# Kernel optimization log

Hardware: AMD Instinct MI355X
Metric: run time of the kernel (lower is better)

## Reference

```python
import jax, jax.numpy as jnp
import numpy as np

L, B, H, IN = 2, 32, 2048, 2048  # layers, batch, hidden, input (=hidden here)


def setup_inputs() -> dict:
    key = jax.random.key(0)
    ks = jax.random.split(key, 8)
    s = 0.02
    return {
        "h0": jax.random.normal(ks[0], (L, B, H), jnp.float32),
        "c0": jax.random.normal(ks[1], (L, B, H), jnp.float32),
        "W_ih": jax.random.normal(ks[2], (L, 4 * H, IN), jnp.float32) * s,
        "W_hh": jax.random.normal(ks[3], (L, 4 * H, H), jnp.float32) * s,
        "b_ih": jax.random.normal(ks[4], (L, 4 * H), jnp.float32) * s,
        "b_hh": jax.random.normal(ks[5], (L, 4 * H), jnp.float32) * s,
        "W_out": jax.random.normal(ks[6], (IN, H), jnp.float32) * s,
        "b_out": jax.random.normal(ks[7], (IN,), jnp.float32) * s,
        "seq_len": 128,
    }


def _lstm_cell(x, h, c, W_ih, W_hh, b_ih, b_hh):
    # gates: [B, 4H]; PyTorch LSTMCell gate order i, f, g, o
    gates = x @ W_ih.T + b_ih + h @ W_hh.T + b_hh
    i, f, g, o = jnp.split(gates, 4, axis=-1)
    c_new = jax.nn.sigmoid(f) * c + jax.nn.sigmoid(i) * jnp.tanh(g)
    h_new = jax.nn.sigmoid(o) * jnp.tanh(c_new)
    return h_new, c_new


def reference(h0, c0, W_ih, W_hh, b_ih, b_hh, W_out, b_out, seq_len):
    batch, hidden = h0.shape[1], h0.shape[2]
    x0 = jnp.zeros((batch, hidden), h0.dtype)

    def step(carry, _):
        x, h, c = carry  # h, c: [L, B, H]
        hs, cs = [], []
        inp = x
        for l in range(h.shape[0]):  # small fixed layer loop
            h_l, c_l = _lstm_cell(inp, h[l], c[l], W_ih[l], W_hh[l], b_ih[l], b_hh[l])
            hs.append(h_l)
            cs.append(c_l)
            inp = h_l
        last_h = hs[-1]
        x_next = last_h @ W_out.T + b_out  # projected feedback
        return (x_next, jnp.stack(hs), jnp.stack(cs)), last_h

    _, out_feats = jax.lax.scan(step, (x0, h0, c0), None, length=seq_len)
    return out_feats  # [seq_len, B, H] (stacked list of per-step top-layer h)
```

## Files before the change

kernel.cpp:

```cpp
#include <hip/hip_runtime.h>


typedef __attribute__((ext_vector_type(8))) short short8;
typedef __attribute__((ext_vector_type(4))) short short4v;
typedef __attribute__((ext_vector_type(4))) float f32x4;

#define MFMA16(a, b, c) __builtin_amdgcn_mfma_f32_16x16x32_bf16((a), (b), (c), 0, 0, 0)
#define GDMA(gp, lp)                                                        \
  __builtin_amdgcn_global_load_lds(                                         \
      (const __attribute__((address_space(1))) unsigned int*)(gp),          \
      (__attribute__((address_space(3))) unsigned int*)(lp), 16, 0, 0)

static constexpr int BATCH = 32;
static constexpr int HID = 2048;
static constexpr int NWG = 256;
static constexpr int NTHR = 512;
static constexpr int BH = BATCH * HID;
static constexpr size_t WMAT = (size_t)8192 * 2048;
static constexpr int LDS_WRING = 0;
static constexpr int LDS_ARING = 32768;
static constexpr int LDS_RED = 98304;
static constexpr int LDS_BYTES = 114688;

#define AT_ADD(p, v) __hip_atomic_fetch_add((p), (v), __ATOMIC_RELAXED, __HIP_MEMORY_SCOPE_AGENT)
#define AT_LD(p) __hip_atomic_load((p), __ATOMIC_RELAXED, __HIP_MEMORY_SCOPE_AGENT)
#define AT_ST(p, v) __hip_atomic_store((p), (v), __ATOMIC_RELAXED, __HIP_MEMORY_SCOPE_AGENT)

__device__ __forceinline__ unsigned short f2bf(float x) {
  unsigned u = __float_as_uint(x);
  u += 0x7FFFu + ((u >> 16) & 1u);
  return (unsigned short)(u >> 16);
}
__device__ __forceinline__ float sigm(float x) { return 1.f / (1.f + __expf(-x)); }
__device__ __forceinline__ float tanh_(float x) {
  float e = __expf(2.f * x);
  return 1.f - 2.f / (e + 1.f);
}

__global__ void cvt_bf16_k(const float* __restrict__ s, unsigned short* __restrict__ d,
                           long n4) {
  long i = blockIdx.x * (long)blockDim.x + threadIdx.x;
  long st = (long)gridDim.x * blockDim.x;
  for (; i < n4; i += st) {
    float4 v = ((const float4*)s)[i];
    short4v o;
    o.x = (short)f2bf(v.x); o.y = (short)f2bf(v.y);
    o.z = (short)f2bf(v.z); o.w = (short)f2bf(v.w);
    ((short4v*)d)[i] = o;
  }
}

__global__ void tcvt_k(const float* __restrict__ src, unsigned short* __restrict__ dst) {
  __shared__ float T[64][65];
  const int jb = blockIdx.x * 64, kb = blockIdx.y * 64;
  const int tid = threadIdx.x;
#pragma unroll
  for (int r = 0; r < 4; ++r) {
    const int row = r * 16 + (tid >> 4), c4 = (tid & 15) * 4;
    float4 v = *(const float4*)&src[(size_t)(jb + row) * 2048 + kb + c4];
    T[row][c4] = v.x; T[row][c4 + 1] = v.y; T[row][c4 + 2] = v.z; T[row][c4 + 3] = v.w;
  }
  __syncthreads();
#pragma unroll
  for (int r = 0; r < 4; ++r) {
    const int k = r * 16 + (tid >> 4), j4 = (tid & 15) * 4;
    short4v o;
    o.x = (short)f2bf(T[j4][k]);     o.y = (short)f2bf(T[j4 + 1][k]);
    o.z = (short)f2bf(T[j4 + 2][k]); o.w = (short)f2bf(T[j4 + 3][k]);
    *(short4v*)&dst[(size_t)(kb + k) * 2048 + jb + j4] = o;
  }
}

__global__ void gemm_pack_k(const unsigned short* __restrict__ A,
                            const unsigned short* __restrict__ Bt,
                            unsigned short* __restrict__ Wfp) {
  __shared__ __align__(16) unsigned short As[128][72], Bs[128][72];
  const int tid = threadIdx.x, wv = tid >> 6, lane = tid & 63;
  const int wm = wv >> 1, wn = wv & 1;
  const int g0 = blockIdx.x * 128, k0 = blockIdx.y * 128;
  f32x4 acc[4][4];
#pragma unroll
  for (int i = 0; i < 4; ++i)
#pragma unroll
    for (int j = 0; j < 4; ++j) acc[i][j] = (f32x4){0.f, 0.f, 0.f, 0.f};

  for (int kt = 0; kt < 32; ++kt) {
#pragma unroll
    for (int rr = 0; rr < 4; ++rr) {
      const int row = rr * 32 + (tid >> 3), c8 = (tid & 7) * 8;
      *(short8*)&As[row][c8] = *(const short8*)&A[(size_t)(g0 + row) * 2048 + kt * 64 + c8];
      *(short8*)&Bs[row][c8] = *(const short8*)&Bt[(size_t)(k0 + row) * 2048 + kt * 64 + c8];
    }
    __syncthreads();
#pragma unroll
    for (int kk = 0; kk < 2; ++kk) {
      short8 af[4], bf[4];
#pragma unroll
      for (int mi = 0; mi < 4; ++mi)
        af[mi] = *(const short8*)&As[wm * 64 + mi * 16 + (lane & 15)][kk * 32 + (lane >> 4) * 8];
#pragma unroll
      for (int ni = 0; ni < 4; ++ni)
        bf[ni] = *(const short8*)&Bs[wn * 64 + ni * 16 + (lane & 15)][kk * 32 + (lane >> 4) * 8];
#pragma unroll
      for (int mi = 0; mi < 4; ++mi)
#pragma unroll
        for (int ni = 0; ni < 4; ++ni)
          acc[mi][ni] = MFMA16(af[mi], bf[ni], acc[mi][ni]);
    }
    __syncthreads();
  }
#pragma unroll
  for (int mi = 0; mi < 4; ++mi)
#pragma unroll
    for (int ni = 0; ni < 4; ++ni)
#pragma unroll
      for (int r = 0; r < 4; ++r) {
        const int g = g0 + wm * 64 + mi * 16 + (lane >> 4) * 4 + r;
        const int k = k0 + wn * 64 + ni * 16 + (lane & 15);
        const int gateblk = g >> 11, gcol = g & 2047;
        const int wgp = gcol >> 3, nn = (gcol & 7) + 8 * (gateblk & 1), tile = gateblk >> 1;
        const int kblk = k >> 5, e = k & 7, lane_p = nn + 16 * ((k >> 3) & 3);
        Wfp[(((size_t)(wgp * 2 + tile) * 64 + kblk) * 64 + lane_p) * 8 + e] =
            f2bf(acc[mi][ni][r]);
      }
}

__global__ void pack_W1_k(const float* __restrict__ src, unsigned short* __restrict__ dst) {
  const int bid = blockIdx.x;
  const int wg = bid >> 1, tile = bid & 1;
  const int tid = threadIdx.x;
  __shared__ __align__(16) unsigned short L[16][2056];
  for (int i = tid; i < 16 * 512; i += 256) {
    const int r = i >> 9, c4 = i & 511;
    const int gr = tile * 4096 + (r < 8 ? wg * 8 + r : 2048 + wg * 8 + r - 8);
    float4 v = ((const float4*)(src + (size_t)gr * 2048))[c4];
    short4v o;
    o.x = (short)f2bf(v.x); o.y = (short)f2bf(v.y);
    o.z = (short)f2bf(v.z); o.w = (short)f2bf(v.w);
    *(short4v*)&L[r][c4 * 4] = o;
  }
  __syncthreads();
  short8* dchunks = (short8*)dst;
  const size_t cbase = (size_t)(wg * 2 + tile) * 64;
  for (int c = tid; c < 4096; c += 256) {
    const int lane = c & 63, kblk = c >> 6;
    const int nn = lane & 15, kb = (lane >> 4) << 3;
    short8 v = *(const short8*)&L[nn][kblk * 32 + kb];
    dchunks[(cbase + kblk) * 64 + lane] = v;
  }
}

__global__ void bias_k(const float* __restrict__ Wih, const float* __restrict__ bout,
                       const float* __restrict__ bih, const float* __restrict__ bhh,
                       float* bA0, float* bAf, float* bB) {
  const int g = blockIdx.x * 8 + (threadIdx.x >> 6);
  const int lane = threadIdx.x & 63;
  float s = 0.f;
  for (int i = 0; i < 32; ++i)
    s += Wih[(size_t)g * 2048 + i * 64 + lane] * bout[i * 64 + lane];
  for (int off = 32; off; off >>= 1) s += __shfl_down(s, off);
  if (lane == 0) {
    const float b0 = bih[g] + bhh[g];
    bA0[g] = b0; bAf[g] = b0 + s;
    bB[g] = bih[8192 + g] + bhh[8192 + g];
  }
}

__global__ void init_k(const float* __restrict__ h0, const float* __restrict__ c0,
                       unsigned short* h0p, unsigned short* h1p, unsigned short* zbuf,
                       float* c0f, float* c1f, unsigned* bar) {
  int i = blockIdx.x * blockDim.x + threadIdx.x;
  if (i < BH) {
    const int e = i & 7, lane = (i >> 3) & 63, kblk = (i >> 9) & 63, mtile = i >> 15;
    const int m = mtile * 16 + (lane & 15);
    const int k = kblk * 32 + ((lane >> 4) << 3) + e;
    h0p[i] = f2bf(h0[m * HID + k]);
    h1p[i] = f2bf(h0[BH + m * HID + k]);
    zbuf[i] = 0;
    c0f[i] = c0[i];
    c1f[i] = c0[BH + i];
  }
  if (i < 320) bar[i] = 0u;
}

__device__ __forceinline__ void grid_barrier(unsigned* bar, int bno) {
  asm volatile("s_waitcnt vmcnt(0)" ::: "memory");
  __syncthreads();
  if (threadIdx.x == 0) {
    __builtin_amdgcn_fence(__ATOMIC_RELEASE, "agent");
    const int g = blockIdx.x >> 5;
    unsigned a = AT_ADD(&bar[g * 32], 1u);
    if (a == (unsigned)(32 * bno - 1)) {
      unsigned m = AT_ADD(&bar[256], 1u);
      if (m == (unsigned)(8 * bno - 1)) AT_ST(&bar[288], (unsigned)bno);
    }
    while (AT_LD(&bar[288]) < (unsigned)bno) __builtin_amdgcn_s_sleep(2);
    __builtin_amdgcn_fence(__ATOMIC_ACQUIRE, "agent");
  }
  __syncthreads();
}

#define PHASE(VARR, WMATP, CBUF, HOUTP, OUTP, BSEL)                               \
  {                                                                               \
    const char* Ab = (const char*)Asrc + ((size_t)(s * 16)) * 1024 + lane * 16;   \
    const char* Wb = (const char*)(WMATP) +                                       \
                     (((size_t)(wg * 2 + 1) * 64) + s * 16) * 1024 + lane * 16;   \
    _Pragma("unroll")                                                             \
    for (int g = 0; g < 4; ++g) {                                                 \
      GDMA(Ab + (size_t)g * 1024,         lds3 + aring + g * 2048);               \
      GDMA(Ab + 65536 + (size_t)g * 1024, lds3 + aring + g * 2048 + 1024);        \
      GDMA(Wb + (size_t)g * 1024,         lds3 + wring + g * 1024);               \
    }                                                                             \
    f32x4 acc00 = {0.f, 0.f, 0.f, 0.f}, acc01 = acc00, acc10 = acc00, acc11 = acc00; \
    _Pragma("unroll")                                                             \
    for (int k = 0; k < 16; ++k) {                                                \
      if (k <= 12)      { asm volatile("s_waitcnt vmcnt(9)" ::: "memory"); }      \
      else if (k == 13) { asm volatile("s_waitcnt vmcnt(6)" ::: "memory"); }      \
      else if (k == 14) { asm volatile("s_waitcnt vmcnt(3)" ::: "memory"); }      \
      else              { asm volatile("s_waitcnt vmcnt(0)" ::: "memory"); }      \
      __builtin_amdgcn_sched_barrier(0);                                          \
      short8 a0 = *(const short8*)(smem + aring + (k & 3) * 2048 + lane * 16);    \
      short8 a1 = *(const short8*)(smem + aring + (k & 3) * 2048 + 1024 + lane * 16); \
      short8 b1 = *(const short8*)(smem + wring + (k & 3) * 1024 + lane * 16);    \
      short8 b0 = VARR[k];                                                        \
      acc00 = MFMA16(a0, b0, acc00); acc01 = MFMA16(a1, b0, acc01);               \
      acc10 = MFMA16(a0, b1, acc10); acc11 = MFMA16(a1, b1, acc11);               \
      __builtin_amdgcn_sched_barrier(0);                                          \
      if (k < 12) {                                                               \
        GDMA(Ab + (size_t)(k + 4) * 1024,         lds3 + aring + ((k + 4) & 3) * 2048); \
        GDMA(Ab + 65536 + (size_t)(k + 4) * 1024, lds3 + aring + ((k + 4) & 3) * 2048 + 1024); \
        GDMA(Wb + (size_t)(k + 4) * 1024,         lds3 + wring + ((k + 4) & 3) * 1024); \
      }                                                                           \
    }                                                                             \
    __syncthreads();                                                              \
    *(f32x4*)&red[((w * 2 + 0) * 64 + lane) * 4] = acc00;                         \
    *(f32x4*)&red[((w * 2 + 1) * 64 + lane) * 4] = acc01;                         \
    __syncthreads();                                                              \
    float gi = 0.f, gf_ = 0.f;                                                    \
    if (tid < 256) {                                                              \
      const int b = tid >> 3, cc = tid & 7, m = b >> 4, br = b & 15;              \
      const int reg = br & 3, lb = (br >> 2) << 4;                                \
      _Pragma("unroll")                                                           \
      for (int ww = 0; ww < 8; ++ww) {                                            \
        gi  += red[((ww * 2 + m) * 64 + lb + cc) * 4 + reg];                      \
        gf_ += red[((ww * 2 + m) * 64 + lb + cc + 8) * 4 + reg];                  \
      }                                                                           \
    }                                                                             \
    __syncthreads();                                                              \
    *(f32x4*)&red[((w * 2 + 0) * 64 + lane) * 4] = acc10;                         \
    *(f32x4*)&red[((w * 2 + 1) * 64 + lane) * 4] = acc11;                         \
    __syncthreads();                                                              \
    if (tid < 256) {                                                              \
      const int b = tid >> 3, cc = tid & 7, m = b >> 4, br = b & 15;              \
      const int reg = br & 3, lb = (br >> 2) << 4;                                \
      float gg = 0.f, go = 0.f;                                                   \
      _Pragma("unroll")                                                           \
      for (int ww = 0; ww < 8; ++ww) {                                            \
        gg += red[((ww * 2 + m) * 64 + lb + cc) * 4 + reg];                       \
        go += red[((ww * 2 + m) * 64 + lb + cc + 8) * 4 + reg];                   \
      }                                                                           \
      const int col = wg * 8 + cc;                                                \
      gi  += (BSEL)[col];                                                         \
      gf_ += (BSEL)[2048 + col];                                                  \
      gg  += (BSEL)[4096 + col];                                                  \
      go  += (BSEL)[6144 + col];                                                  \
      const float iv = sigm(gi), fv = sigm(gf_), gv = tanh_(gg), ov = sigm(go);   \
      const float cold = (CBUF)[b * HID + col];                                   \
      const float cnew = fv * cold + iv * gv;                                     \
      const float hnew = ov * tanh_(cnew);                                        \
      (CBUF)[b * HID + col] = cnew;                                               \
      const int kblk = col >> 5, lh = (col >> 3) & 3, e = col & 7;                \
      const int lane_p = (b & 15) | (lh << 4), mt = b >> 4;                       \
      (HOUTP)[((size_t)(mt * 64 + kblk) * 64 + lane_p) * 8 + e] = f2bf(hnew);     \
      if (OUTP) ((float*)(OUTP))[b * HID + col] = hnew;                           \
    }                                                                             \
  }

__global__ __launch_bounds__(NTHR, 2) void lstm_persist(
    const unsigned short* __restrict__ Wfp, const unsigned short* __restrict__ Wh0p,
    const unsigned short* __restrict__ Wi1p, const unsigned short* __restrict__ Wh1p,
    const float* __restrict__ bA0, const float* __restrict__ bAf,
    const float* __restrict__ bB,
    unsigned short* h0p, unsigned short* h1p, const unsigned short* zbuf,
    float* c0f, float* c1f, float* __restrict__ out, int T, unsigned* bar) {
  extern __shared__ __align__(16) char smem[];
  auto* lds3 = (__attribute__((address_space(3))) char*)smem;
  float* red = (float*)(smem + LDS_RED);
  const int wg = blockIdx.x, tid = threadIdx.x;
  const int w = tid >> 6, lane = tid & 63;
  const int p = w >> 2, s = w & 3;
  const int wring = LDS_WRING + w * 4096;
  const int aring = LDS_ARING + w * 8192;
  const unsigned short* M0 = p ? Wh0p : Wfp;
  const unsigned short* M1 = p ? Wh1p : Wi1p;

  short8 vA[16], vB[16];
  {
    const short8* m0c = (const short8*)M0;
    const short8* m1c = (const short8*)M1;
#pragma unroll
    for (int c = 0; c < 16; ++c)
      vA[c] = m0c[(((size_t)(wg * 2 + 0) * 64) + s * 16 + c) * 64 + lane];
#pragma unroll
    for (int c = 0; c < 16; ++c)
      vB[c] = m1c[(((size_t)(wg * 2 + 0) * 64) + s * 16 + c) * 64 + lane];
  }
#pragma unroll
  for (int c = 0; c < 16; ++c) {
    asm volatile("" : "+v"(vA[c]));
    asm volatile("" : "+v"(vB[c]));
  }
  asm volatile("s_waitcnt vmcnt(0)" ::: "memory");
  __builtin_amdgcn_sched_barrier(0);

  int bno = 1;
  for (int t = 0; t < T; ++t) {
    const int par = t & 1;
    {
      const unsigned short* Asrc =
          (p == 0) ? ((t == 0) ? zbuf : h1p + par * BH) : (h0p + par * BH);
      const float* bsel = (t == 0) ? bA0 : bAf;
      PHASE(vA, M0, c0f, h0p + (par ^ 1) * BH, (float*)nullptr, bsel)
    }
    grid_barrier(bar, bno++);
    {
      const unsigned short* Asrc = (p == 0) ? (h0p + (par ^ 1) * BH) : (h1p + par * BH);
      PHASE(vB, M1, c1f, h1p + (par ^ 1) * BH, out + (size_t)t * BH, bB)
    }
    grid_barrier(bar, bno++);
  }
}

extern "C" void kernel_launch(void* const* d_in, const int* in_sizes, int n_in,
                              void* d_out, int out_size, void* d_ws, size_t ws_size,
                              hipStream_t stream) {
  const float* h0 = (const float*)d_in[0];
  const float* c0 = (const float*)d_in[1];
  const float* Wih = (const float*)d_in[2];
  const float* Whh = (const float*)d_in[3];
  const float* bih = (const float*)d_in[4];
  const float* bhh = (const float*)d_in[5];
  const float* Wout = (const float*)d_in[6];
  const float* bout = (const float*)d_in[7];
  float* out = (float*)d_out;
  const int T = out_size / BH;

  unsigned short* Wfp = (unsigned short*)d_ws;
  unsigned short* Wh0p = Wfp + WMAT;
  unsigned short* Wi1p = Wfp + 2 * WMAT;
  unsigned short* Wh1p = Wfp + 3 * WMAT;
  unsigned short* tmpA = Wi1p;
  unsigned short* WoutT = Wh1p;
  unsigned short* S = Wfp + 4 * WMAT;
  unsigned short* h0p = S;
  unsigned short* h1p = S + 131072;
  unsigned short* zbuf = S + 262144;
  float* F = (float*)(S + 327680);
  float* c0f = F;
  float* c1f = F + 65536;
  float* bA0 = F + 131072;
  float* bAf = F + 139264;
  float* bB = F + 147456;
  unsigned* bar = (unsigned*)(F + 155648);

  cvt_bf16_k<<<2048, 256, 0, stream>>>(Wih, tmpA, (long)(WMAT / 4));
  tcvt_k<<<dim3(32, 32), 256, 0, stream>>>(Wout, WoutT);
  gemm_pack_k<<<dim3(64, 16), 256, 0, stream>>>(tmpA, WoutT, Wfp);
  pack_W1_k<<<512, 256, 0, stream>>>(Whh, Wh0p);
  pack_W1_k<<<512, 256, 0, stream>>>(Wih + WMAT, Wi1p);
  pack_W1_k<<<512, 256, 0, stream>>>(Whh + WMAT, Wh1p);
  bias_k<<<1024, 512, 0, stream>>>(Wih, bout, bih, bhh, bA0, bAf, bB);
  init_k<<<256, 256, 0, stream>>>(h0, c0, h0p, h1p, zbuf, c0f, c1f, bar);

  (void)hipFuncSetAttribute((const void*)lstm_persist,
                            hipFuncAttributeMaxDynamicSharedMemorySize, LDS_BYTES);
  lstm_persist<<<NWG, NTHR, LDS_BYTES, stream>>>(Wfp, Wh0p, Wi1p, Wh1p,
                                                 bA0, bAf, bB,
                                                 h0p, h1p, zbuf, c0f, c1f, out, T, bar);
}
```

Before: 4.321 ms.

## Stream weights via LDS ring, keep activations in registers, cache part of phase-A weights in LDS

Register-resident weight fragments (vA/vB, 32 short8 per lane) are dropped. Twelve of the sixteen phase-A weight k-slices are now kept resident in LDS, and all other weight tiles are streamed through a 6-slot per-wave LDS ring with global_load_lds. The h activation tiles are read directly from global memory into registers instead of going through LDS. This frees a large block of VGPRs and raises LDS use to 144 KB, but phase B now re-streams its full weight tile from global/L2 on every step. Activation loads also become direct global loads inside the MFMA loop, which could expose their latency.

```diff
diff --git a/kernel.cpp b/kernel.cpp
--- a/kernel.cpp
+++ b/kernel.cpp
@@ -17,10 +17,8 @@
 static constexpr int NTHR = 512;
 static constexpr int BH = BATCH * HID;
 static constexpr size_t WMAT = (size_t)8192 * 2048;
-static constexpr int LDS_WRING = 0;
-static constexpr int LDS_ARING = 32768;
-static constexpr int LDS_RED = 98304;
-static constexpr int LDS_BYTES = 114688;
+static constexpr int LDS_RES = 49152;
+static constexpr int LDS_BYTES = 147456;
 
 #define AT_ADD(p, v) __hip_atomic_fetch_add((p), (v), __ATOMIC_RELAXED, __HIP_MEMORY_SCOPE_AGENT)
 #define AT_LD(p) __hip_atomic_load((p), __ATOMIC_RELAXED, __HIP_MEMORY_SCOPE_AGENT)
@@ -200,80 +198,116 @@
   __syncthreads();
 }
 
-#define PHASE(VARR, WMATP, CBUF, HOUTP, OUTP, BSEL)                               \
+#define EPILOG(CBUF, HOUTP, OUTP, BSEL)                                           \
+  __syncthreads();                                                                \
+  *(f32x4*)&red[((w * 2 + 0) * 64 + lane) * 4] = acc00;                           \
+  *(f32x4*)&red[((w * 2 + 1) * 64 + lane) * 4] = acc01;                           \
+  __syncthreads();                                                                \
+  float gi = 0.f, gf_ = 0.f;                                                      \
+  if (tid < 256) {                                                                \
+    const int b = tid >> 3, cc = tid & 7, m = b >> 4, br = b & 15;                \
+    const int reg = br & 3, lb = (br >> 2) << 4;                                  \
+    _Pragma("unroll")                                                             \
+    for (int ww = 0; ww < 8; ++ww) {                                              \
+      gi  += red[((ww * 2 + m) * 64 + lb + cc) * 4 + reg];                        \
+      gf_ += red[((ww * 2 + m) * 64 + lb + cc + 8) * 4 + reg];                    \
+    }                                                                             \
+  }                                                                               \
+  __syncthreads();                                                                \
+  *(f32x4*)&red[((w * 2 + 0) * 64 + lane) * 4] = acc10;                           \
+  *(f32x4*)&red[((w * 2 + 1) * 64 + lane) * 4] = acc11;                           \
+  __syncthreads();                                                                \
+  if (tid < 256) {                                                                \
+    const int b = tid >> 3, cc = tid & 7, m = b >> 4, br = b & 15;                \
+    const int reg = br & 3, lb = (br >> 2) << 4;                                  \
+    float gg = 0.f, go = 0.f;                                                     \
+    _Pragma("unroll")                                                             \
+    for (int ww = 0; ww < 8; ++ww) {                                              \
+      gg += red[((ww * 2 + m) * 64 + lb + cc) * 4 + reg];                         \
+      go += red[((ww * 2 + m) * 64 + lb + cc + 8) * 4 + reg];                     \
+    }                                                                             \
+    const int col = wg * 8 + cc;                                                  \
+    gi  += (BSEL)[col];                                                           \
+    gf_ += (BSEL)[2048 + col];                                                    \
+    gg  += (BSEL)[4096 + col];                                                    \
+    go  += (BSEL)[6144 + col];                                                    \
+    const float iv = sigm(gi), fv = sigm(gf_), gv = tanh_(gg), ov = sigm(go);     \
+    const float cold = (CBUF)[b * HID + col];                                     \
+    const float cnew = fv * cold + iv * gv;                                       \
+    const float hnew = ov * tanh_(cnew);                                          \
+    (CBUF)[b * HID + col] = cnew;                                                 \
+    const int kblk = col >> 5, lh = (col >> 3) & 3, e = col & 7;                  \
+    const int lane_p = (b & 15) | (lh << 4), mt = b >> 4;                         \
+    (HOUTP)[((size_t)(mt * 64 + kblk) * 64 + lane_p) * 8 + e] = f2bf(hnew);       \
+    if (OUTP) ((float*)(OUTP))[b * HID + col] = hnew;                             \
+  }
+
+#define A_IT(i)                                                                   \
+  ((i) < 12 ? (WAt1 + (size_t)(i) * 1024)                                         \
+            : ((((i) - 12) & 1) ? (WAt1 + (size_t)(12 + (((i) - 12) >> 1)) * 1024)\
+                                : (WAt0 + (size_t)(12 + (((i) - 12) >> 1)) * 1024)))
+
+#define PHASE_A(CBUF, HOUTP, OUTP, BSEL)                                          \
   {                                                                               \
-    const char* Ab = (const char*)Asrc + ((size_t)(s * 16)) * 1024 + lane * 16;   \
-    const char* Wb = (const char*)(WMATP) +                                       \
-                     (((size_t)(wg * 2 + 1) * 64) + s * 16) * 1024 + lane * 16;   \
-    _Pragma("unroll")                                                             \
-    for (int g = 0; g < 4; ++g) {                                                 \
-      GDMA(Ab + (size_t)g * 1024,         lds3 + aring + g * 2048);               \
-      GDMA(Ab + 65536 + (size_t)g * 1024, lds3 + aring + g * 2048 + 1024);        \
-      GDMA(Wb + (size_t)g * 1024,         lds3 + wring + g * 1024);               \
-    }                                                                             \
+    const short8* pA0 = (const short8*)Asrc + (s * 16) * 64 + lane;               \
+    const short8* pA1 = pA0 + 64 * 64;                                            \
+    _Pragma("unroll")                                                             \
+    for (int i = 0; i < 6; ++i) GDMA(A_IT(i), lds3 + ring + (i % 6) * 1024);      \
     f32x4 acc00 = {0.f, 0.f, 0.f, 0.f}, acc01 = acc00, acc10 = acc00, acc11 = acc00; \
     _Pragma("unroll")                                                             \
     for (int k = 0; k < 16; ++k) {                                                \
-      if (k <= 12)      { asm volatile("s_waitcnt vmcnt(9)" ::: "memory"); }      \
-      else if (k == 13) { asm volatile("s_waitcnt vmcnt(6)" ::: "memory"); }      \
-      else if (k == 14) { asm volatile("s_waitcnt vmcnt(3)" ::: "memory"); }      \
+      if (k < 12)       { asm volatile("s_waitcnt vmcnt(5)" ::: "memory"); }      \
+      else if (k <= 13) { asm volatile("s_waitcnt vmcnt(4)" ::: "memory"); }      \
+      else if (k == 14) { asm volatile("s_waitcnt vmcnt(2)" ::: "memory"); }      \
       else              { asm volatile("s_waitcnt vmcnt(0)" ::: "memory"); }      \
       __builtin_amdgcn_sched_barrier(0);                                          \
-      short8 a0 = *(const short8*)(smem + aring + (k & 3) * 2048 + lane * 16);    \
-      short8 a1 = *(const short8*)(smem + aring + (k & 3) * 2048 + 1024 + lane * 16); \
-      short8 b1 = *(const short8*)(smem + wring + (k & 3) * 1024 + lane * 16);    \
-      short8 b0 = VARR[k];                                                        \
+      short8 b0 = (k < 12)                                                        \
+          ? *(const short8*)(smem + res + k * 1024 + lane * 16)                   \
+          : *(const short8*)(smem + ring + ((12 + 2 * (k - 12)) % 6) * 1024 + lane * 16); \
+      short8 b1 = (k < 12)                                                        \
+          ? *(const short8*)(smem + ring + (k % 6) * 1024 + lane * 16)            \
+          : *(const short8*)(smem + ring + ((13 + 2 * (k - 12)) % 6) * 1024 + lane * 16); \
+      short8 a0 = pA0[k * 64];                                                    \
+      short8 a1 = pA1[k * 64];                                                    \
       acc00 = MFMA16(a0, b0, acc00); acc01 = MFMA16(a1, b0, acc01);               \
       acc10 = MFMA16(a0, b1, acc10); acc11 = MFMA16(a1, b1, acc11);               \
-      __builtin_amdgcn_sched_barrier(0);                                          \
-      if (k < 12) {                                                               \
-        GDMA(Ab + (size_t)(k + 4) * 1024,         lds3 + aring + ((k + 4) & 3) * 2048); \
-        GDMA(Ab + 65536 + (size_t)(k + 4) * 1024, lds3 + aring + ((k + 4) & 3) * 2048 + 1024); \
-        GDMA(Wb + (size_t)(k + 4) * 1024,         lds3 + wring + ((k + 4) & 3) * 1024); \
+      if (k <= 11) { GDMA(A_IT(k + 6), lds3 + ring + ((k + 6) % 6) * 1024); }     \
+      if (k == 12) {                                                              \
+        GDMA(A_IT(18), lds3 + ring + 0 * 1024);                                   \
+        GDMA(A_IT(19), lds3 + ring + 1 * 1024);                                   \
       }                                                                           \
     }                                                                             \
-    __syncthreads();                                                              \
-    *(f32x4*)&red[((w * 2 + 0) * 64 + lane) * 4] = acc00;                         \
-    *(f32x4*)&red[((w * 2 + 1) * 64 + lane) * 4] = acc01;                         \
-    __syncthreads();                                                              \
-    float gi = 0.f, gf_ = 0.f;                                                    \
-    if (tid < 256) {                                                              \
-      const int b = tid >> 3, cc = tid & 7, m = b >> 4, br = b & 15;              \
-      const int reg = br & 3, lb = (br >> 2) << 4;                                \
-      _Pragma("unroll")                                                           \
-      for (int ww = 0; ww < 8; ++ww) {                                            \
-        gi  += red[((ww * 2 + m) * 64 + lb + cc) * 4 + reg];                      \
-        gf_ += red[((ww * 2 + m) * 64 + lb + cc + 8) * 4 + reg];                  \
+    EPILOG(CBUF, HOUTP, OUTP, BSEL)                                               \
+  }
+
+#define B_IT(i)                                                                   \
+  (((i) & 1) ? (WBt1 + (size_t)((i) >> 1) * 1024) : (WBt0 + (size_t)((i) >> 1) * 1024))
+
+#define PHASE_B(CBUF, HOUTP, OUTP, BSEL)                                          \
+  {                                                                               \
+    const short8* pA0 = (const short8*)Asrc + (s * 16) * 64 + lane;               \
+    const short8* pA1 = pA0 + 64 * 64;                                            \
+    _Pragma("unroll")                                                             \
+    for (int i = 0; i < 6; ++i) GDMA(B_IT(i), lds3 + ring + (i % 6) * 1024);      \
+    f32x4 acc00 = {0.f, 0.f, 0.f, 0.f}, acc01 = acc00, acc10 = acc00, acc11 = acc00; \
+    _Pragma("unroll")                                                             \
+    for (int k = 0; k < 16; ++k) {                                                \
+      if (k <= 13)      { asm volatile("s_waitcnt vmcnt(4)" ::: "memory"); }      \
+      else if (k == 14) { asm volatile("s_waitcnt vmcnt(2)" ::: "memory"); }      \
+      else              { asm volatile("s_waitcnt vmcnt(0)" ::: "memory"); }      \
+      __builtin_amdgcn_sched_barrier(0);                                          \
+      short8 b0 = *(const short8*)(smem + ring + ((2 * k) % 6) * 1024 + lane * 16);     \
+      short8 b1 = *(const short8*)(smem + ring + ((2 * k + 1) % 6) * 1024 + lane * 16); \
+      short8 a0 = pA0[k * 64];                                                    \
+      short8 a1 = pA1[k * 64];                                                    \
+      acc00 = MFMA16(a0, b0, acc00); acc01 = MFMA16(a1, b0, acc01);               \
+      acc10 = MFMA16(a0, b1, acc10); acc11 = MFMA16(a1, b1, acc11);               \
+      if (k <= 12) {                                                              \
+        GDMA(B_IT(2 * k + 6), lds3 + ring + ((2 * k + 6) % 6) * 1024);            \
+        GDMA(B_IT(2 * k + 7), lds3 + ring + ((2 * k + 7) % 6) * 1024);            \
       }                                                                           \
     }                                                                             \
-    __syncthreads();                                                              \
-    *(f32x4*)&red[((w * 2 + 0) * 64 + lane) * 4] = acc10;                         \
-    *(f32x4*)&red[((w * 2 + 1) * 64 + lane) * 4] = acc11;                         \
-    __syncthreads();                                                              \
-    if (tid < 256) {                                                              \
-      const int b = tid >> 3, cc = tid & 7, m = b >> 4, br = b & 15;              \
-      const int reg = br & 3, lb = (br >> 2) << 4;                                \
-      float gg = 0.f, go = 0.f;                                                   \
-      _Pragma("unroll")                                                           \
-      for (int ww = 0; ww < 8; ++ww) {                                            \
-        gg += red[((ww * 2 + m) * 64 + lb + cc) * 4 + reg];                       \
-        go += red[((ww * 2 + m) * 64 + lb + cc + 8) * 4 + reg];                   \
-      }                                                                           \
-      const int col = wg * 8 + cc;                                                \
-      gi  += (BSEL)[col];                                                         \
-      gf_ += (BSEL)[2048 + col];                                                  \
-      gg  += (BSEL)[4096 + col];                                                  \
-      go  += (BSEL)[6144 + col];                                                  \
-      const float iv = sigm(gi), fv = sigm(gf_), gv = tanh_(gg), ov = sigm(go);   \
-      const float cold = (CBUF)[b * HID + col];                                   \
-      const float cnew = fv * cold + iv * gv;                                     \
-      const float hnew = ov * tanh_(cnew);                                        \
-      (CBUF)[b * HID + col] = cnew;                                               \
-      const int kblk = col >> 5, lh = (col >> 3) & 3, e = col & 7;                \
-      const int lane_p = (b & 15) | (lh << 4), mt = b >> 4;                       \
-      (HOUTP)[((size_t)(mt * 64 + kblk) * 64 + lane_p) * 8 + e] = f2bf(hnew);     \
-      if (OUTP) ((float*)(OUTP))[b * HID + col] = hnew;                           \
-    }                                                                             \
+    EPILOG(CBUF, HOUTP, OUTP, BSEL)                                               \
   }
 
 __global__ __launch_bounds__(NTHR, 2) void lstm_persist(
@@ -285,33 +319,23 @@
     float* c0f, float* c1f, float* __restrict__ out, int T, unsigned* bar) {
   extern __shared__ __align__(16) char smem[];
   auto* lds3 = (__attribute__((address_space(3))) char*)smem;
-  float* red = (float*)(smem + LDS_RED);
+  float* red = (float*)smem;
   const int wg = blockIdx.x, tid = threadIdx.x;
   const int w = tid >> 6, lane = tid & 63;
   const int p = w >> 2, s = w & 3;
-  const int wring = LDS_WRING + w * 4096;
-  const int aring = LDS_ARING + w * 8192;
+  const int ring = w * 6144;
+  const int res = LDS_RES + w * 12288;
   const unsigned short* M0 = p ? Wh0p : Wfp;
   const unsigned short* M1 = p ? Wh1p : Wi1p;
-
-  short8 vA[16], vB[16];
-  {
-    const short8* m0c = (const short8*)M0;
-    const short8* m1c = (const short8*)M1;
-#pragma unroll
-    for (int c = 0; c < 16; ++c)
-      vA[c] = m0c[(((size_t)(wg * 2 + 0) * 64) + s * 16 + c) * 64 + lane];
-#pragma unroll
-    for (int c = 0; c < 16; ++c)
-      vB[c] = m1c[(((size_t)(wg * 2 + 0) * 64) + s * 16 + c) * 64 + lane];
-  }
-#pragma unroll
-  for (int c = 0; c < 16; ++c) {
-    asm volatile("" : "+v"(vA[c]));
-    asm volatile("" : "+v"(vB[c]));
-  }
+  const char* WAt0 = (const char*)M0 + (((size_t)(wg * 2 + 0) * 64) + s * 16) * 1024 + lane * 16;
+  const char* WAt1 = (const char*)M0 + (((size_t)(wg * 2 + 1) * 64) + s * 16) * 1024 + lane * 16;
+  const char* WBt0 = (const char*)M1 + (((size_t)(wg * 2 + 0) * 64) + s * 16) * 1024 + lane * 16;
+  const char* WBt1 = (const char*)M1 + (((size_t)(wg * 2 + 1) * 64) + s * 16) * 1024 + lane * 16;
+
+#pragma unroll
+  for (int c = 0; c < 12; ++c) GDMA(WAt0 + (size_t)c * 1024, lds3 + res + c * 1024);
   asm volatile("s_waitcnt vmcnt(0)" ::: "memory");
-  __builtin_amdgcn_sched_barrier(0);
+  __syncthreads();
 
   int bno = 1;
   for (int t = 0; t < T; ++t) {
@@ -320,12 +344,12 @@
       const unsigned short* Asrc =
           (p == 0) ? ((t == 0) ? zbuf : h1p + par * BH) : (h0p + par * BH);
       const float* bsel = (t == 0) ? bA0 : bAf;
-      PHASE(vA, M0, c0f, h0p + (par ^ 1) * BH, (float*)nullptr, bsel)
+      PHASE_A(c0f, h0p + (par ^ 1) * BH, (float*)nullptr, bsel)
     }
     grid_barrier(bar, bno++);
     {
       const unsigned short* Asrc = (p == 0) ? (h0p + (par ^ 1) * BH) : (h1p + par * BH);
-      PHASE(vB, M1, c1f, h1p + (par ^ 1) * BH, out + (size_t)t * BH, bB)
+      PHASE_B(c1f, h1p + (par ^ 1) * BH, out + (size_t)t * BH, bB)
     }
     grid_barrier(bar, bno++);
   }
```

Result: slower. 4.790 ms (+10.8%).
